# Kernel optimization log

Hardware: AMD Instinct MI355X
Metric: run time of the kernel (lower is better)

The kernel has to match this reference:

```python
import jax, jax.numpy as jnp
import numpy as np

EPS = 1e-8  # torch F.cosine_similarity eps


def setup_inputs() -> dict:
    key = jax.random.key(0)
    B, CAP, CD, CTX = 32, 32768, 64, 64
    ks = jax.random.split(key, 9)
    inp = {
        "query_content": jax.random.normal(ks[0], (B, CD), jnp.float32),
        "query_context": jax.random.normal(ks[1], (B, CTX), jnp.float32),
        "memory_content": 0.1 * jax.random.normal(ks[2], (CAP, CD), jnp.float32),
        "memory_contexts": 0.1 * jax.random.normal(ks[3], (CAP, CTX), jnp.float32),
        "memory_freshness": jnp.ones((CAP,), jnp.float32),
        "W1": jax.random.normal(ks[4], (2 * CD, CD), jnp.float32) / np.sqrt(2 * CD),
        "b1": 0.01 * jax.random.normal(ks[5], (CD,), jnp.float32),
        "W2": jax.random.normal(ks[6], (CD, 1), jnp.float32) / np.sqrt(CD),
        "b2": 0.01 * jax.random.normal(ks[7], (1,), jnp.float32),
        "top_k": 16,
    }
    return inp


def reference(query_content, query_context, memory_content, memory_contexts,
              memory_freshness, W1, b1, W2, b2, top_k):
    B, CD = query_content.shape
    # similarity_calculator MLP over all (query, memory) pairs.
    # Linear on concat([q, m]) == q @ W1[:CD] + m @ W1[CD:]  (avoids the concat).
    q_part = query_content @ W1[:CD]            # [B, CD]
    m_part = memory_content @ W1[CD:]           # [CAP, CD]
    h = jax.nn.relu(q_part[:, None, :] + m_part[None, :, :] + b1)  # [B, CAP, CD]
    content_sim = jax.nn.sigmoid(jnp.einsum('bch,h->bc', h, W2[:, 0]) + b2[0])  # [B, CAP]

    # cosine similarity between query_context and each stored context
    qn = query_context / jnp.maximum(jnp.linalg.norm(query_context, axis=-1, keepdims=True), EPS)
    mn = memory_contexts / jnp.maximum(jnp.linalg.norm(memory_contexts, axis=-1, keepdims=True), EPS)
    context_sim = qn @ mn.T                      # [B, CAP]

    time_weights = memory_freshness              # time_mask is all-ones in source
    final = 0.5 * content_sim + 0.3 * context_sim + 0.2 * time_weights[None, :]

    top_similarities, top_indices = jax.lax.top_k(final, top_k)   # [B, k]
    retrieved_content = memory_content[top_indices]               # [B, k, CD]
    retrieved_time_weights = time_weights[top_indices]            # [B, k]
    return (retrieved_content, top_similarities, retrieved_time_weights)
```

## Files before the change

kernel.cpp:

```cpp
#include <hip/hip_runtime.h>
#include <math.h>

#define CAP   32768
#define NB    32
#define CD    64
#define ROWS  64
#define NBLK  (CAP / ROWS)
#define TOPK  16
#define CEPS  1e-8f

#define WS_QP    0
#define WS_QN    2048
#define WS_FINAL 4096

#define PITCH 68

#define CHUNK 2048
#define NCHUNK (CAP / CHUNK)

__global__ __launch_bounds__(64) void prep_kernel(
    const float* __restrict__ qc,
    const float* __restrict__ qctx,
    const float* __restrict__ W1,
    const float* __restrict__ b1,
    float* __restrict__ ws)
{
    const int b = blockIdx.x;
    const int j = threadIdx.x;

    float acc = b1[j];
    #pragma unroll 8
    for (int i = 0; i < 64; ++i)
        acc = fmaf(qc[b * 64 + i], W1[i * 64 + j], acc);
    ws[WS_QP + b * 64 + j] = acc;

    float x = qctx[b * 64 + j];
    float ss = x * x;
    ss += __shfl_xor(ss, 1,  64);
    ss += __shfl_xor(ss, 2,  64);
    ss += __shfl_xor(ss, 4,  64);
    ss += __shfl_xor(ss, 8,  64);
    ss += __shfl_xor(ss, 16, 64);
    ss += __shfl_xor(ss, 32, 64);
    float nrm = fmaxf(sqrtf(ss), CEPS);
    ws[WS_QN + b * 64 + j] = x / nrm;
}

__device__ __forceinline__ void acc_pair(const float4 qp, const float4 qn,
                                         const float4 m, const float4 xv,
                                         const float4 w2, float& a1, float& a2)
{
    a1 = fmaf(fmaxf(qp.x + m.x, 0.f), w2.x, a1);
    a1 = fmaf(fmaxf(qp.y + m.y, 0.f), w2.y, a1);
    a1 = fmaf(fmaxf(qp.z + m.z, 0.f), w2.z, a1);
    a1 = fmaf(fmaxf(qp.w + m.w, 0.f), w2.w, a1);
    a2 = fmaf(qn.x, xv.x, a2);
    a2 = fmaf(qn.y, xv.y, a2);
    a2 = fmaf(qn.z, xv.z, a2);
    a2 = fmaf(qn.w, xv.w, a2);
}

__global__ __launch_bounds__(256) void score_kernel(
    const float* __restrict__ mcont,
    const float* __restrict__ mctx,
    const float* __restrict__ fresh,
    const float* __restrict__ W1,
    const float* __restrict__ W2,
    const float* __restrict__ b2,
    float* __restrict__ ws)
{
    __shared__ float s_mc[ROWS * PITCH];
    __shared__ float s_mx[ROWS * PITCH];
    __shared__ float s_mp[ROWS * PITCH];
    __shared__ float s_qp[NB * PITCH];
    __shared__ float s_qn[NB * PITCH];
    __shared__ float s_w2[64];
    __shared__ float s_base[ROWS];
    __shared__ float s_inv[ROWS];

    const int tid = threadIdx.x;
    const int lane = tid & 63;
    const int C0 = blockIdx.x * ROWS;

    const float4* g_mc = (const float4*)(mcont + (size_t)C0 * 64);
    const float4* g_mx = (const float4*)(mctx  + (size_t)C0 * 64);
    #pragma unroll
    for (int t = tid; t < ROWS * 16; t += 256) {
        int r = t >> 4, c4 = t & 15;
        *(float4*)&s_mc[r * PITCH + c4 * 4] = g_mc[t];
        *(float4*)&s_mx[r * PITCH + c4 * 4] = g_mx[t];
    }
    const float4* g_qp = (const float4*)(ws + WS_QP);
    const float4* g_qn = (const float4*)(ws + WS_QN);
    #pragma unroll
    for (int t = tid; t < NB * 16; t += 256) {
        int r = t >> 4, c4 = t & 15;
        *(float4*)&s_qp[r * PITCH + c4 * 4] = g_qp[t];
        *(float4*)&s_qn[r * PITCH + c4 * 4] = g_qn[t];
    }
    if (tid < 64) {
        s_w2[tid]   = W2[tid];
        s_base[tid] = 0.2f * fresh[C0 + tid];
    }

    float w1c[64];
    #pragma unroll
    for (int i = 0; i < 64; ++i)
        w1c[i] = W1[(64 + i) * 64 + lane];

    __syncthreads();

    const int wv = tid >> 6;
    for (int r = 0; r < 16; ++r) {
        const int c = wv * 16 + r;
        const float* row = &s_mc[c * PITCH];
        float acc = 0.f;
        #pragma unroll
        for (int i4 = 0; i4 < 16; ++i4) {
            float4 m = *(const float4*)&row[i4 * 4];
            acc = fmaf(m.x, w1c[4 * i4 + 0], acc);
            acc = fmaf(m.y, w1c[4 * i4 + 1], acc);
            acc = fmaf(m.z, w1c[4 * i4 + 2], acc);
            acc = fmaf(m.w, w1c[4 * i4 + 3], acc);
        }
        s_mp[c * PITCH + lane] = acc;

        float x = s_mx[c * PITCH + lane];
        float ss = x * x;
        ss += __shfl_xor(ss, 1,  64);
        ss += __shfl_xor(ss, 2,  64);
        ss += __shfl_xor(ss, 4,  64);
        ss += __shfl_xor(ss, 8,  64);
        ss += __shfl_xor(ss, 16, 64);
        ss += __shfl_xor(ss, 32, 64);
        if (lane == 0)
            s_inv[c] = 0.3f / fmaxf(sqrtf(ss), CEPS);
    }
    __syncthreads();

    const int bq = (tid & 15) << 1;
    const int cq = (tid >> 4) << 2;
    float a1[2][4] = {{0.f}}, a2[2][4] = {{0.f}};

    #pragma unroll 4
    for (int j4 = 0; j4 < 16; ++j4) {
        const int jo = j4 * 4;
        float4 w2v  = *(const float4*)&s_w2[jo];
        float4 qp0  = *(const float4*)&s_qp[ bq      * PITCH + jo];
        float4 qp1  = *(const float4*)&s_qp[(bq + 1) * PITCH + jo];
        float4 qn0  = *(const float4*)&s_qn[ bq      * PITCH + jo];
        float4 qn1  = *(const float4*)&s_qn[(bq + 1) * PITCH + jo];
        #pragma unroll
        for (int ci = 0; ci < 4; ++ci) {
            float4 mv = *(const float4*)&s_mp[(cq + ci) * PITCH + jo];
            float4 xv = *(const float4*)&s_mx[(cq + ci) * PITCH + jo];
            acc_pair(qp0, qn0, mv, xv, w2v, a1[0][ci], a2[0][ci]);
            acc_pair(qp1, qn1, mv, xv, w2v, a1[1][ci], a2[1][ci]);
        }
    }

    const float b2v = b2[0];
    #pragma unroll
    for (int bi = 0; bi < 2; ++bi) {
        #pragma unroll
        for (int ci = 0; ci < 4; ++ci) {
            const int b = bq + bi, c = cq + ci;
            float logit = a1[bi][ci] + b2v;
            float sig = 0.5f / (1.f + expf(-logit));
            float fin = sig + a2[bi][ci] * s_inv[c] + s_base[c];
            ws[WS_FINAL + (size_t)b * CAP + C0 + c] = fin;
        }
    }
}

__global__ __launch_bounds__(256) void topk_part1(float* __restrict__ ws)
{
    __shared__ float cval[2][8];
    __shared__ int   cidx[2][8];

    const int tid = threadIdx.x;
    const int wv  = tid >> 6;
    const int lane = tid & 63;
    const int b = blockIdx.y;
    float* row = ws + WS_FINAL + (size_t)b * CAP;
    const int cbase = blockIdx.x * CHUNK;
    const int tbase = cbase + tid * 8;

    float4 v0 = *(const float4*)&row[tbase];
    float4 v1 = *(const float4*)&row[tbase + 4];
    float v[8] = {v0.x, v0.y, v0.z, v0.w, v1.x, v1.y, v1.z, v1.w};

    for (int k = 0; k < TOPK; ++k) {
        float bv = v[0]; int bj = 0;
        #pragma unroll
        for (int j = 1; j < 8; ++j)
            if (v[j] > bv) { bv = v[j]; bj = j; }
        int bi = tbase + bj;

        #pragma unroll
        for (int off = 1; off < 64; off <<= 1) {
            float ov = __shfl_xor(bv, off, 64);
            int   oi = __shfl_xor(bi, off, 64);
            if (ov > bv || (ov == bv && oi < bi)) { bv = ov; bi = oi; }
        }
        if (lane == 0) { cval[k & 1][wv] = bv; cidx[k & 1][wv] = bi; }
        __syncthreads();

        float Wv = cval[k & 1][0]; int Wi = cidx[k & 1][0];
        #pragma unroll
        for (int w = 1; w < 4; ++w) {
            float ov = cval[k & 1][w]; int oi = cidx[k & 1][w];
            if (ov > Wv || (ov == Wv && oi < Wi)) { Wv = ov; Wi = oi; }
        }
        if (tid == 0) {
            row[cbase + k]        = Wv;
            row[cbase + TOPK + k] = __int_as_float(Wi);
        }
        #pragma unroll
        for (int j = 0; j < 8; ++j)
            if (Wi == tbase + j) v[j] = -INFINITY;
    }
}

__global__ __launch_bounds__(256) void topk_part2(
    const float* __restrict__ mcont,
    const float* __restrict__ fresh,
    const float* __restrict__ ws,
    float* __restrict__ out)
{
    __shared__ float cval[2][8];
    __shared__ int   cidx[2][8];
    __shared__ int   swin[TOPK];

    const int tid = threadIdx.x;
    const int wv  = tid >> 6;
    const int lane = tid & 63;
    const int b = blockIdx.x;
    const float* row = ws + WS_FINAL + (size_t)b * CAP;

    float* out_content = out;
    float* out_sim     = out + NB * TOPK * 64;
    float* out_tw      = out + NB * TOPK * 64 + NB * TOPK;

    const int chunk = tid >> 4, slot = tid & 15;
    float val = row[chunk * CHUNK + slot];
    int   idx = __float_as_int(row[chunk * CHUNK + TOPK + slot]);

    for (int k = 0; k < TOPK; ++k) {
        float bv = val; int bi = idx;
        #pragma unroll
        for (int off = 1; off < 64; off <<= 1) {
            float ov = __shfl_xor(bv, off, 64);
            int   oi = __shfl_xor(bi, off, 64);
            if (ov > bv || (ov == bv && oi < bi)) { bv = ov; bi = oi; }
        }
        if (lane == 0) { cval[k & 1][wv] = bv; cidx[k & 1][wv] = bi; }
        __syncthreads();

        float Wv = cval[k & 1][0]; int Wi = cidx[k & 1][0];
        #pragma unroll
        for (int w = 1; w < 4; ++w) {
            float ov = cval[k & 1][w]; int oi = cidx[k & 1][w];
            if (ov > Wv || (ov == Wv && oi < Wi)) { Wv = ov; Wi = oi; }
        }
        if (tid == 0) {
            out_sim[b * TOPK + k] = Wv;
            out_tw [b * TOPK + k] = fresh[Wi];
            swin[k] = Wi;
        }
        if (idx == Wi) val = -INFINITY;
    }
    __syncthreads();

    for (int t = tid; t < TOPK * 64; t += 256)
        out_content[(size_t)b * TOPK * 64 + t] =
            mcont[(size_t)swin[t >> 6] * 64 + (t & 63)];
}

extern "C" void kernel_launch(void* const* d_in, const int* in_sizes, int n_in,
                              void* d_out, int out_size, void* d_ws, size_t ws_size,
                              hipStream_t stream) {
    const float* qc    = (const float*)d_in[0];
    const float* qctx  = (const float*)d_in[1];
    const float* mcont = (const float*)d_in[2];
    const float* mctx  = (const float*)d_in[3];
    const float* fresh = (const float*)d_in[4];
    const float* W1    = (const float*)d_in[5];
    const float* b1    = (const float*)d_in[6];
    const float* W2    = (const float*)d_in[7];
    const float* b2    = (const float*)d_in[8];
    float* out = (float*)d_out;
    float* ws  = (float*)d_ws;

    prep_kernel<<<NB, 64, 0, stream>>>(qc, qctx, W1, b1, ws);
    score_kernel<<<NBLK, 256, 0, stream>>>(mcont, mctx, fresh, W1, W2, b2, ws);
    topk_part1<<<dim3(NCHUNK, NB), 256, 0, stream>>>(ws);
    topk_part2<<<NB, 256, 0, stream>>>(mcont, fresh, ws, out);
}
```

Baseline: 146.2 us.

## Use single-wave top-k selection, split FMA accumulators, and stage score stores

Measured after the change: 144.4 us. No clear change (-1.2%).

```diff
diff --git a/kernel.cpp b/kernel.cpp
--- a/kernel.cpp
+++ b/kernel.cpp
@@ -28,11 +28,15 @@
     const int b = blockIdx.x;
     const int j = threadIdx.x;
 
-    float acc = b1[j];
-    #pragma unroll 8
-    for (int i = 0; i < 64; ++i)
-        acc = fmaf(qc[b * 64 + i], W1[i * 64 + j], acc);
-    ws[WS_QP + b * 64 + j] = acc;
+    float a0 = b1[j], a1 = 0.f, a2 = 0.f, a3 = 0.f;
+    #pragma unroll
+    for (int i = 0; i < 64; i += 4) {
+        a0 = fmaf(qc[b * 64 + i + 0], W1[(i + 0) * 64 + j], a0);
+        a1 = fmaf(qc[b * 64 + i + 1], W1[(i + 1) * 64 + j], a1);
+        a2 = fmaf(qc[b * 64 + i + 2], W1[(i + 2) * 64 + j], a2);
+        a3 = fmaf(qc[b * 64 + i + 3], W1[(i + 3) * 64 + j], a3);
+    }
+    ws[WS_QP + b * 64 + j] = (a0 + a1) + (a2 + a3);
 
     float x = qctx[b * 64 + j];
     float ss = x * x;
@@ -114,16 +118,23 @@
     for (int r = 0; r < 16; ++r) {
         const int c = wv * 16 + r;
         const float* row = &s_mc[c * PITCH];
-        float acc = 0.f;
-        #pragma unroll
-        for (int i4 = 0; i4 < 16; ++i4) {
-            float4 m = *(const float4*)&row[i4 * 4];
-            acc = fmaf(m.x, w1c[4 * i4 + 0], acc);
-            acc = fmaf(m.y, w1c[4 * i4 + 1], acc);
-            acc = fmaf(m.z, w1c[4 * i4 + 2], acc);
-            acc = fmaf(m.w, w1c[4 * i4 + 3], acc);
-        }
-        s_mp[c * PITCH + lane] = acc;
+        float a0 = 0.f, a1 = 0.f, a2 = 0.f, a3 = 0.f;
+        #pragma unroll
+        for (int i4 = 0; i4 < 16; i4 += 4) {
+            float4 m0 = *(const float4*)&row[(i4 + 0) * 4];
+            float4 m1 = *(const float4*)&row[(i4 + 1) * 4];
+            float4 m2 = *(const float4*)&row[(i4 + 2) * 4];
+            float4 m3 = *(const float4*)&row[(i4 + 3) * 4];
+            a0 = fmaf(m0.x, w1c[4*i4+ 0], a0); a0 = fmaf(m0.y, w1c[4*i4+ 1], a0);
+            a0 = fmaf(m0.z, w1c[4*i4+ 2], a0); a0 = fmaf(m0.w, w1c[4*i4+ 3], a0);
+            a1 = fmaf(m1.x, w1c[4*i4+ 4], a1); a1 = fmaf(m1.y, w1c[4*i4+ 5], a1);
+            a1 = fmaf(m1.z, w1c[4*i4+ 6], a1); a1 = fmaf(m1.w, w1c[4*i4+ 7], a1);
+            a2 = fmaf(m2.x, w1c[4*i4+ 8], a2); a2 = fmaf(m2.y, w1c[4*i4+ 9], a2);
+            a2 = fmaf(m2.z, w1c[4*i4+10], a2); a2 = fmaf(m2.w, w1c[4*i4+11], a2);
+            a3 = fmaf(m3.x, w1c[4*i4+12], a3); a3 = fmaf(m3.y, w1c[4*i4+13], a3);
+            a3 = fmaf(m3.z, w1c[4*i4+14], a3); a3 = fmaf(m3.w, w1c[4*i4+15], a3);
+        }
+        s_mp[c * PITCH + lane] = (a0 + a1) + (a2 + a3);
 
         float x = s_mx[c * PITCH + lane];
         float ss = x * x;
@@ -167,35 +178,41 @@
             const int b = bq + bi, c = cq + ci;
             float logit = a1[bi][ci] + b2v;
             float sig = 0.5f / (1.f + expf(-logit));
-            float fin = sig + a2[bi][ci] * s_inv[c] + s_base[c];
-            ws[WS_FINAL + (size_t)b * CAP + C0 + c] = fin;
-        }
-    }
-}
-
-__global__ __launch_bounds__(256) void topk_part1(float* __restrict__ ws)
-{
-    __shared__ float cval[2][8];
-    __shared__ int   cidx[2][8];
-
-    const int tid = threadIdx.x;
-    const int wv  = tid >> 6;
-    const int lane = tid & 63;
+            s_mc[b * PITCH + c] = sig + a2[bi][ci] * s_inv[c] + s_base[c];
+        }
+    }
+    __syncthreads();
+
+    #pragma unroll
+    for (int it = 0; it < 2; ++it) {
+        int idx = it * 256 + tid;
+        int b = idx >> 4, c4 = idx & 15;
+        *(float4*)&ws[WS_FINAL + (size_t)b * CAP + C0 + c4 * 4] =
+            *(const float4*)&s_mc[b * PITCH + c4 * 4];
+    }
+}
+
+__global__ __launch_bounds__(64) void topk_part1(float* __restrict__ ws)
+{
+    const int lane = threadIdx.x;
     const int b = blockIdx.y;
     float* row = ws + WS_FINAL + (size_t)b * CAP;
     const int cbase = blockIdx.x * CHUNK;
-    const int tbase = cbase + tid * 8;
-
-    float4 v0 = *(const float4*)&row[tbase];
-    float4 v1 = *(const float4*)&row[tbase + 4];
-    float v[8] = {v0.x, v0.y, v0.z, v0.w, v1.x, v1.y, v1.z, v1.w};
+
+    float v[32];
+    #pragma unroll
+    for (int j = 0; j < 32; ++j)
+        v[j] = row[cbase + j * 64 + lane];
+
+    float outv = 0.f;
+    int   outi = 0;
 
     for (int k = 0; k < TOPK; ++k) {
         float bv = v[0]; int bj = 0;
         #pragma unroll
-        for (int j = 1; j < 8; ++j)
+        for (int j = 1; j < 32; ++j)
             if (v[j] > bv) { bv = v[j]; bj = j; }
-        int bi = tbase + bj;
+        int bi = cbase + bj * 64 + lane;
 
         #pragma unroll
         for (int off = 1; off < 64; off <<= 1) {
@@ -203,38 +220,29 @@
             int   oi = __shfl_xor(bi, off, 64);
             if (ov > bv || (ov == bv && oi < bi)) { bv = ov; bi = oi; }
         }
-        if (lane == 0) { cval[k & 1][wv] = bv; cidx[k & 1][wv] = bi; }
-        __syncthreads();
-
-        float Wv = cval[k & 1][0]; int Wi = cidx[k & 1][0];
-        #pragma unroll
-        for (int w = 1; w < 4; ++w) {
-            float ov = cval[k & 1][w]; int oi = cidx[k & 1][w];
-            if (ov > Wv || (ov == Wv && oi < Wi)) { Wv = ov; Wi = oi; }
-        }
-        if (tid == 0) {
-            row[cbase + k]        = Wv;
-            row[cbase + TOPK + k] = __int_as_float(Wi);
-        }
-        #pragma unroll
-        for (int j = 0; j < 8; ++j)
-            if (Wi == tbase + j) v[j] = -INFINITY;
-    }
-}
-
-__global__ __launch_bounds__(256) void topk_part2(
+        if (lane == k) { outv = bv; outi = bi; }
+
+        int rel = bi - cbase;
+        bool mine = ((rel & 63) == lane);
+        int wj = rel >> 6;
+        #pragma unroll
+        for (int j = 0; j < 32; ++j)
+            if (mine && wj == j) v[j] = -INFINITY;
+    }
+
+    if (lane < TOPK) {
+        row[cbase + lane]        = outv;
+        row[cbase + TOPK + lane] = __int_as_float(outi);
+    }
+}
+
+__global__ __launch_bounds__(64) void topk_part2(
     const float* __restrict__ mcont,
     const float* __restrict__ fresh,
     const float* __restrict__ ws,
     float* __restrict__ out)
 {
-    __shared__ float cval[2][8];
-    __shared__ int   cidx[2][8];
-    __shared__ int   swin[TOPK];
-
-    const int tid = threadIdx.x;
-    const int wv  = tid >> 6;
-    const int lane = tid & 63;
+    const int lane = threadIdx.x;
     const int b = blockIdx.x;
     const float* row = ws + WS_FINAL + (size_t)b * CAP;
 
@@ -242,39 +250,44 @@
     float* out_sim     = out + NB * TOPK * 64;
     float* out_tw      = out + NB * TOPK * 64 + NB * TOPK;
 
-    const int chunk = tid >> 4, slot = tid & 15;
-    float val = row[chunk * CHUNK + slot];
-    int   idx = __float_as_int(row[chunk * CHUNK + TOPK + slot]);
-
+    const int chunk = lane & 15;
+    const int s0 = lane >> 4;
+    float v[4]; int iv[4];
+    #pragma unroll
+    for (int s = 0; s < 4; ++s) {
+        v[s]  = row[chunk * CHUNK + s0 + 4 * s];
+        iv[s] = __float_as_int(row[chunk * CHUNK + TOPK + s0 + 4 * s]);
+    }
+
+    float wval = 0.f; int widx = 0;
     for (int k = 0; k < TOPK; ++k) {
-        float bv = val; int bi = idx;
+        float bv = v[0]; int bi = iv[0];
+        #pragma unroll
+        for (int s = 1; s < 4; ++s)
+            if (v[s] > bv || (v[s] == bv && iv[s] < bi)) { bv = v[s]; bi = iv[s]; }
         #pragma unroll
         for (int off = 1; off < 64; off <<= 1) {
             float ov = __shfl_xor(bv, off, 64);
             int   oi = __shfl_xor(bi, off, 64);
             if (ov > bv || (ov == bv && oi < bi)) { bv = ov; bi = oi; }
         }
-        if (lane == 0) { cval[k & 1][wv] = bv; cidx[k & 1][wv] = bi; }
-        __syncthreads();
-
-        float Wv = cval[k & 1][0]; int Wi = cidx[k & 1][0];
-        #pragma unroll
-        for (int w = 1; w < 4; ++w) {
-            float ov = cval[k & 1][w]; int oi = cidx[k & 1][w];
-            if (ov > Wv || (ov == Wv && oi < Wi)) { Wv = ov; Wi = oi; }
-        }
-        if (tid == 0) {
-            out_sim[b * TOPK + k] = Wv;
-            out_tw [b * TOPK + k] = fresh[Wi];
-            swin[k] = Wi;
-        }
-        if (idx == Wi) val = -INFINITY;
-    }
-    __syncthreads();
-
-    for (int t = tid; t < TOPK * 64; t += 256)
-        out_content[(size_t)b * TOPK * 64 + t] =
-            mcont[(size_t)swin[t >> 6] * 64 + (t & 63)];
+        if (lane == k) { wval = bv; widx = bi; }
+        #pragma unroll
+        for (int s = 0; s < 4; ++s)
+            if (iv[s] == bi) v[s] = -INFINITY;
+    }
+
+    if (lane < TOPK) {
+        out_sim[b * TOPK + lane] = wval;
+        out_tw [b * TOPK + lane] = fresh[widx];
+    }
+
+    #pragma unroll
+    for (int r = 0; r < TOPK; ++r) {
+        int wi = __shfl(widx, r, 64);
+        out_content[(size_t)b * TOPK * 64 + r * 64 + lane] =
+            mcont[(size_t)wi * 64 + lane];
+    }
 }
 
 extern "C" void kernel_launch(void* const* d_in, const int* in_sizes, int n_in,
@@ -294,6 +307,6 @@
 
     prep_kernel<<<NB, 64, 0, stream>>>(qc, qctx, W1, b1, ws);
     score_kernel<<<NBLK, 256, 0, stream>>>(mcont, mctx, fresh, W1, W2, b2, ws);
-    topk_part1<<<dim3(NCHUNK, NB), 256, 0, stream>>>(ws);
-    topk_part2<<<NB, 256, 0, stream>>>(mcont, fresh, ws, out);
-}
+    topk_part1<<<dim3(NCHUNK, NB), 64, 0, stream>>>(ws);
+    topk_part2<<<NB, 64, 0, stream>>>(mcont, fresh, ws, out);
+}
```
